# Optimization experiments

Measured on AMD Instinct MI355X. Metric: run time of the kernel, lower is better.

Reference implementation:

```python
import jax, jax.numpy as jnp
import numpy as np

N = 8192      # number of tokens/nodes
D = 256       # out_dim
E = N - 1     # one dependency triple per non-root node
ALPHA = 0.2   # LeakyReLU negative slope


def setup_inputs() -> dict:
    key = jax.random.key(0)
    k1, k2, k3, k4 = jax.random.split(key, 4)
    x = jax.random.normal(k1, (N, D), jnp.float32)
    W = jax.random.normal(k2, (D, D), jnp.float32) / np.sqrt(D)      # nn.Linear(out,out,bias=False).weight
    a = jax.random.normal(k3, (2 * D,), jnp.float32) / np.sqrt(2 * D)  # nn.Linear(2*out,1,bias=False).weight
    # each node 1..N-1 is a dependent exactly once -> h_dict keys are [0,1,...,N-1] in order
    dep = jnp.arange(1, N, dtype=jnp.int32)
    # each governor appears at most once -> each e_tensor row is softmaxed exactly once
    gov = jax.random.permutation(k4, N)[:E].astype(jnp.int32)
    return {"x": x, "W": W, "a": a, "dep": dep, "gov": gov}


def reference(x, W, a, dep, gov):
    Nn, Dd = x.shape
    neg_big = jnp.asarray(-1e18, x.dtype)
    Hx = x @ W.T  # self.weight(x[i]) for every node, [N, D]
    # per-edge attention logit: attn_weight(cat(W x_gov, W x_dep))
    s = jnp.concatenate([Hx[gov], Hx[dep]], axis=-1) @ a  # [E]
    # dense e_tensor exactly as in the module
    e = jnp.zeros((Nn, Nn), x.dtype).at[gov, dep].set(s)
    # rows belonging to a governor get masked softmax; other rows untouched
    gov_mask = jnp.zeros((Nn,), bool).at[gov].set(True)
    masked = jnp.where(e > 0, e, neg_big)
    sm = jax.nn.softmax(masked, axis=1)
    attn = jnp.where(gov_mask[:, None], sm, e)
    # self_loop/h_dict init: h[dep] = W x[gov]; node 0 stays zeros
    h = jnp.zeros((Nn, Dd), x.dtype).at[dep].set(Hx[gov])
    # aggregation: h[gov] += attn[gov, dep] * W x[dep]
    coef = attn[gov, dep]  # [E]
    h = h + jax.ops.segment_sum(coef[:, None] * Hx[dep], gov, num_segments=Nn)
    return jax.nn.leaky_relu(h, ALPHA)
```

## Files before the change

### kernel.cpp

```cpp
#include <hip/hip_runtime.h>
#include <hip/hip_bf16.h>

#define NN 8192
#define DD 256
#define EE (NN - 1)

typedef __attribute__((ext_vector_type(8))) short bf16x8;
typedef __attribute__((ext_vector_type(4))) float f32x4;

__device__ inline unsigned short f2bf(float f) {
  return __builtin_bit_cast(unsigned short, __float2bfloat16(f));
}

__global__ __launch_bounds__(1024) void prep(
    const float* __restrict__ W, const float* __restrict__ a,
    const int* __restrict__ gov,
    float* __restrict__ u, float* __restrict__ v, int* __restrict__ inv) {
  const int t = threadIdx.x;
  const int k = t & 255, part = t >> 8;

  for (int i = t; i < NN; i += 1024) inv[i] = -1;
  __syncthreads();
  for (int e = t; e < EE; e += 1024) inv[gov[e]] = e;

  float up = 0.f, vp = 0.f;
  const int j0 = part * 64;
#pragma unroll 4
  for (int j = j0; j < j0 + 64; ++j) {
    float w = W[(size_t)j * DD + k];
    up = fmaf(a[j], w, up);
    vp = fmaf(a[DD + j], w, vp);
  }
  __shared__ float redu[4][256], redv[4][256];
  redu[part][k] = up; redv[part][k] = vp;
  __syncthreads();
  if (t < 256) {
    u[t] = redu[0][t] + redu[1][t] + redu[2][t] + redu[3][t];
    v[t] = redv[0][t] + redv[1][t] + redv[2][t] + redv[3][t];
  }
}

__global__ __launch_bounds__(256) void pq_kernel(
    const float* __restrict__ x, const float* __restrict__ u,
    const float* __restrict__ v, float* __restrict__ p, float* __restrict__ q) {
  const int wid = threadIdx.x >> 6, lane = threadIdx.x & 63;
  const int row = blockIdx.x * 4 + wid;
  const float4 xv = *(const float4*)&x[(size_t)row * DD + lane * 4];
  const float4 uv = *(const float4*)&u[lane * 4];
  const float4 vv = *(const float4*)&v[lane * 4];
  float ps = xv.x * uv.x + xv.y * uv.y + xv.z * uv.z + xv.w * uv.w;
  float qs = xv.x * vv.x + xv.y * vv.y + xv.z * vv.z + xv.w * vv.w;
#pragma unroll
  for (int off = 32; off; off >>= 1) {
    ps += __shfl_xor(ps, off);
    qs += __shfl_xor(qs, off);
  }
  if (lane == 0) { p[row] = ps; q[row] = qs; }
}

__global__ __launch_bounds__(256) void combine(
    const float* __restrict__ x, const float* __restrict__ p,
    const float* __restrict__ q, const int* __restrict__ gov,
    const int* __restrict__ inv, unsigned short* __restrict__ y) {
  const int sub = threadIdx.x >> 6, lane = threadIdx.x & 63;
  const int j = blockIdx.x * 4 + sub;

  float4 h = make_float4(0.f, 0.f, 0.f, 0.f);
  if (j > 0) {
    const int g = gov[j - 1];
    h = *(const float4*)&x[(size_t)g * DD + lane * 4];
  }
  const int e2 = inv[j];
  if (e2 >= 0) {
    const int d = e2 + 1;
    const float4 xd = *(const float4*)&x[(size_t)d * DD + lane * 4];
    const float s = p[j] + q[d];
    const float coef = (s > 0.f) ? 1.f : (1.f / 8192.f);
    h.x = fmaf(coef, xd.x, h.x);
    h.y = fmaf(coef, xd.y, h.y);
    h.z = fmaf(coef, xd.z, h.z);
    h.w = fmaf(coef, xd.w, h.w);
  }
  ushort4 pk;
  pk.x = f2bf(h.x); pk.y = f2bf(h.y); pk.z = f2bf(h.z); pk.w = f2bf(h.w);
  *(ushort4*)&y[(size_t)j * DD + lane * 4] = pk;
}

#define BM 64
#define BN 64
#define BK 32
#define LDAB 40

__global__ __launch_bounds__(256) void gemm_out(
    const unsigned short* __restrict__ Y, const float* __restrict__ W,
    float* __restrict__ out) {
  __shared__ unsigned short As[BM][LDAB];
  __shared__ unsigned short Bs[BN][LDAB];
  const int t = threadIdx.x;
  const int bm = blockIdx.x * BM, bn = blockIdx.y * BN;
  const int lane = t & 63, wid = t >> 6;
  const int wr = wid >> 1, wc = wid & 1;
  const int l15 = lane & 15, l4 = lane >> 4;
  const int srow = t >> 2, sseg = t & 3;

  f32x4 acc[2][2] = {};

  for (int k0 = 0; k0 < DD; k0 += BK) {
    {
      ushort4 w0 = *(const ushort4*)&Y[(size_t)(bm + srow) * DD + k0 + sseg * 8];
      ushort4 w1 = *(const ushort4*)&Y[(size_t)(bm + srow) * DD + k0 + sseg * 8 + 4];
      *(ushort4*)&As[srow][sseg * 8] = w0;
      *(ushort4*)&As[srow][sseg * 8 + 4] = w1;
    }
    {
      const float* src = &W[(size_t)(bn + srow) * DD + k0 + sseg * 8];
      float4 f0 = *(const float4*)src;
      float4 f1 = *(const float4*)(src + 4);
      ushort4 p0, p1;
      p0.x = f2bf(f0.x); p0.y = f2bf(f0.y); p0.z = f2bf(f0.z); p0.w = f2bf(f0.w);
      p1.x = f2bf(f1.x); p1.y = f2bf(f1.y); p1.z = f2bf(f1.z); p1.w = f2bf(f1.w);
      *(ushort4*)&Bs[srow][sseg * 8] = p0;
      *(ushort4*)&Bs[srow][sseg * 8 + 4] = p1;
    }
    __syncthreads();

    bf16x8 af[2], bfr[2];
#pragma unroll
    for (int mf = 0; mf < 2; ++mf)
      af[mf] = *(const bf16x8*)&As[wr * 32 + mf * 16 + l15][l4 * 8];
#pragma unroll
    for (int nf = 0; nf < 2; ++nf)
      bfr[nf] = *(const bf16x8*)&Bs[wc * 32 + nf * 16 + l15][l4 * 8];
#pragma unroll
    for (int mf = 0; mf < 2; ++mf)
#pragma unroll
      for (int nf = 0; nf < 2; ++nf)
        acc[mf][nf] = __builtin_amdgcn_mfma_f32_16x16x32_bf16(
            af[mf], bfr[nf], acc[mf][nf], 0, 0, 0);
    __syncthreads();
  }

#pragma unroll
  for (int mf = 0; mf < 2; ++mf)
#pragma unroll
    for (int nf = 0; nf < 2; ++nf)
#pragma unroll
      for (int r = 0; r < 4; ++r) {
        const int row = bm + wr * 32 + mf * 16 + l4 * 4 + r;
        const int col = bn + wc * 32 + nf * 16 + l15;
        float hval = acc[mf][nf][r];
        out[(size_t)row * DD + col] = (hval >= 0.f) ? hval : 0.2f * hval;
      }
}

extern "C" void kernel_launch(void* const* d_in, const int* in_sizes, int n_in,
                              void* d_out, int out_size, void* d_ws, size_t ws_size,
                              hipStream_t stream) {
  const float* x = (const float*)d_in[0];
  const float* W = (const float*)d_in[1];
  const float* a = (const float*)d_in[2];
  const int* gov = (const int*)d_in[4];

  float* p = (float*)d_ws;
  float* q = p + NN;
  float* u = q + NN;
  float* v = u + DD;
  int* inv = (int*)(v + DD);
  unsigned short* y = (unsigned short*)(inv + NN);

  hipLaunchKernelGGL(prep, dim3(1), dim3(1024), 0, stream, W, a, gov, u, v, inv);
  hipLaunchKernelGGL(pq_kernel, dim3(NN / 4), dim3(256), 0, stream, x, u, v, p, q);
  hipLaunchKernelGGL(combine, dim3(NN / 4), dim3(256), 0, stream,
                     x, p, q, gov, inv, y);
  hipLaunchKernelGGL(gemm_out, dim3(NN / BM, DD / BN), dim3(256), 0, stream,
                     y, W, (float*)d_out);
}
```

Baseline: 96.94 us.

## Fuse all four stages into one cooperative persistent kernel with grid syncs

Replaces the four separate launches (prep, pq, combine, gemm) with a single cooperative kernel of 512 blocks that steps through the phases using grid.sync. The u/v projection is now split across 64 blocks with a two-level reduction instead of one 1024-thread block, which shortens the serial prep step. The p/q dot products are computed inline in the combine phase, so the separate p/q pass and its arrays go away. The aim is to cut launch gaps and the single-block bottleneck, at the cost of three grid-wide barriers and a fixed grid that must fit fully resident on the device.

```diff
diff --git a/kernel.cpp b/kernel.cpp
--- a/kernel.cpp
+++ b/kernel.cpp
@@ -1,9 +1,14 @@
 #include <hip/hip_runtime.h>
 #include <hip/hip_bf16.h>
+#include <hip/hip_cooperative_groups.h>
+
+namespace cg = cooperative_groups;
 
 #define NN 8192
 #define DD 256
 #define EE (NN - 1)
+#define NB 512
+#define NT 256
 
 typedef __attribute__((ext_vector_type(8))) short bf16x8;
 typedef __attribute__((ext_vector_type(4))) float f32x4;
@@ -12,145 +17,144 @@
   return __builtin_bit_cast(unsigned short, __float2bfloat16(f));
 }
 
-__global__ __launch_bounds__(1024) void prep(
-    const float* __restrict__ W, const float* __restrict__ a,
-    const int* __restrict__ gov,
-    float* __restrict__ u, float* __restrict__ v, int* __restrict__ inv) {
-  const int t = threadIdx.x;
-  const int k = t & 255, part = t >> 8;
-
-  for (int i = t; i < NN; i += 1024) inv[i] = -1;
-  __syncthreads();
-  for (int e = t; e < EE; e += 1024) inv[gov[e]] = e;
-
-  float up = 0.f, vp = 0.f;
-  const int j0 = part * 64;
-#pragma unroll 4
-  for (int j = j0; j < j0 + 64; ++j) {
-    float w = W[(size_t)j * DD + k];
-    up = fmaf(a[j], w, up);
-    vp = fmaf(a[DD + j], w, vp);
-  }
-  __shared__ float redu[4][256], redv[4][256];
-  redu[part][k] = up; redv[part][k] = vp;
-  __syncthreads();
-  if (t < 256) {
-    u[t] = redu[0][t] + redu[1][t] + redu[2][t] + redu[3][t];
-    v[t] = redv[0][t] + redv[1][t] + redv[2][t] + redv[3][t];
-  }
-}
-
-__global__ __launch_bounds__(256) void pq_kernel(
-    const float* __restrict__ x, const float* __restrict__ u,
-    const float* __restrict__ v, float* __restrict__ p, float* __restrict__ q) {
-  const int wid = threadIdx.x >> 6, lane = threadIdx.x & 63;
-  const int row = blockIdx.x * 4 + wid;
-  const float4 xv = *(const float4*)&x[(size_t)row * DD + lane * 4];
-  const float4 uv = *(const float4*)&u[lane * 4];
-  const float4 vv = *(const float4*)&v[lane * 4];
-  float ps = xv.x * uv.x + xv.y * uv.y + xv.z * uv.z + xv.w * uv.w;
-  float qs = xv.x * vv.x + xv.y * vv.y + xv.z * vv.z + xv.w * vv.w;
-#pragma unroll
-  for (int off = 32; off; off >>= 1) {
-    ps += __shfl_xor(ps, off);
-    qs += __shfl_xor(qs, off);
-  }
-  if (lane == 0) { p[row] = ps; q[row] = qs; }
-}
-
-__global__ __launch_bounds__(256) void combine(
-    const float* __restrict__ x, const float* __restrict__ p,
-    const float* __restrict__ q, const int* __restrict__ gov,
-    const int* __restrict__ inv, unsigned short* __restrict__ y) {
-  const int sub = threadIdx.x >> 6, lane = threadIdx.x & 63;
-  const int j = blockIdx.x * 4 + sub;
-
-  float4 h = make_float4(0.f, 0.f, 0.f, 0.f);
-  if (j > 0) {
-    const int g = gov[j - 1];
-    h = *(const float4*)&x[(size_t)g * DD + lane * 4];
-  }
-  const int e2 = inv[j];
-  if (e2 >= 0) {
-    const int d = e2 + 1;
-    const float4 xd = *(const float4*)&x[(size_t)d * DD + lane * 4];
-    const float s = p[j] + q[d];
-    const float coef = (s > 0.f) ? 1.f : (1.f / 8192.f);
-    h.x = fmaf(coef, xd.x, h.x);
-    h.y = fmaf(coef, xd.y, h.y);
-    h.z = fmaf(coef, xd.z, h.z);
-    h.w = fmaf(coef, xd.w, h.w);
-  }
-  ushort4 pk;
-  pk.x = f2bf(h.x); pk.y = f2bf(h.y); pk.z = f2bf(h.z); pk.w = f2bf(h.w);
-  *(ushort4*)&y[(size_t)j * DD + lane * 4] = pk;
-}
-
 #define BM 64
 #define BN 64
-#define BK 32
 #define LDAB 40
 
-__global__ __launch_bounds__(256) void gemm_out(
-    const unsigned short* __restrict__ Y, const float* __restrict__ W,
+__global__ __launch_bounds__(NT, 2) void fused(
+    const float* __restrict__ x, const float* __restrict__ W,
+    const float* __restrict__ a, const int* __restrict__ gov,
+    float* __restrict__ pu, float* __restrict__ pv,
+    float* __restrict__ u, float* __restrict__ v,
+    int* __restrict__ inv, unsigned short* __restrict__ y,
     float* __restrict__ out) {
+  cg::grid_group grid = cg::this_grid();
+  const int blk = blockIdx.x, t = threadIdx.x;
+
   __shared__ unsigned short As[BM][LDAB];
   __shared__ unsigned short Bs[BN][LDAB];
-  const int t = threadIdx.x;
-  const int bm = blockIdx.x * BM, bn = blockIdx.y * BN;
-  const int lane = t & 63, wid = t >> 6;
-  const int wr = wid >> 1, wc = wid & 1;
-  const int l15 = lane & 15, l4 = lane >> 4;
-  const int srow = t >> 2, sseg = t & 3;
 
-  f32x4 acc[2][2] = {};
+  if (blk < 64) {
+    float su = 0.f, sv = 0.f;
+    const int j0 = blk * 4;
+#pragma unroll
+    for (int jj = 0; jj < 4; ++jj) {
+      float w = W[(size_t)(j0 + jj) * DD + t];
+      su = fmaf(a[j0 + jj], w, su);
+      sv = fmaf(a[DD + j0 + jj], w, sv);
+    }
+    pu[blk * DD + t] = su;
+    pv[blk * DD + t] = sv;
+  } else if (blk < 96) {
+    inv[(blk - 64) * 256 + t] = -1;
+  }
+  grid.sync();
 
-  for (int k0 = 0; k0 < DD; k0 += BK) {
-    {
-      ushort4 w0 = *(const ushort4*)&Y[(size_t)(bm + srow) * DD + k0 + sseg * 8];
-      ushort4 w1 = *(const ushort4*)&Y[(size_t)(bm + srow) * DD + k0 + sseg * 8 + 4];
-      *(ushort4*)&As[srow][sseg * 8] = w0;
-      *(ushort4*)&As[srow][sseg * 8 + 4] = w1;
+  if (blk == 0) {
+    float su = 0.f, sv = 0.f;
+#pragma unroll 8
+    for (int b = 0; b < 64; ++b) {
+      su += pu[b * DD + t];
+      sv += pv[b * DD + t];
     }
-    {
-      const float* src = &W[(size_t)(bn + srow) * DD + k0 + sseg * 8];
-      float4 f0 = *(const float4*)src;
-      float4 f1 = *(const float4*)(src + 4);
-      ushort4 p0, p1;
-      p0.x = f2bf(f0.x); p0.y = f2bf(f0.y); p0.z = f2bf(f0.z); p0.w = f2bf(f0.w);
-      p1.x = f2bf(f1.x); p1.y = f2bf(f1.y); p1.z = f2bf(f1.z); p1.w = f2bf(f1.w);
-      *(ushort4*)&Bs[srow][sseg * 8] = p0;
-      *(ushort4*)&Bs[srow][sseg * 8 + 4] = p1;
+    u[t] = su;
+    v[t] = sv;
+  } else if (blk >= 96 && blk < 128) {
+    const int e = (blk - 96) * 256 + t;
+    if (e < EE) inv[gov[e]] = e;
+  }
+  grid.sync();
+
+  {
+    const int wid = t >> 6, lane = t & 63;
+    const float4 uv = *(const float4*)&u[lane * 4];
+    const float4 vv = *(const float4*)&v[lane * 4];
+#pragma unroll
+    for (int r = 0; r < 4; ++r) {
+      const int j = blk * 16 + wid * 4 + r;
+      float4 h = make_float4(0.f, 0.f, 0.f, 0.f);
+      if (j > 0) {
+        const int g = gov[j - 1];
+        h = *(const float4*)&x[(size_t)g * DD + lane * 4];
+      }
+      const int e2 = inv[j];
+      if (e2 >= 0) {
+        const int d = e2 + 1;
+        const float4 xj = *(const float4*)&x[(size_t)j * DD + lane * 4];
+        const float4 xd = *(const float4*)&x[(size_t)d * DD + lane * 4];
+        float s = xj.x * uv.x + xj.y * uv.y + xj.z * uv.z + xj.w * uv.w +
+                  xd.x * vv.x + xd.y * vv.y + xd.z * vv.z + xd.w * vv.w;
+#pragma unroll
+        for (int off = 32; off; off >>= 1) s += __shfl_xor(s, off);
+        const float coef = (s > 0.f) ? 1.f : (1.f / 8192.f);
+        h.x = fmaf(coef, xd.x, h.x);
+        h.y = fmaf(coef, xd.y, h.y);
+        h.z = fmaf(coef, xd.z, h.z);
+        h.w = fmaf(coef, xd.w, h.w);
+      }
+      ushort4 pk;
+      pk.x = f2bf(h.x); pk.y = f2bf(h.y); pk.z = f2bf(h.z); pk.w = f2bf(h.w);
+      *(ushort4*)&y[(size_t)j * DD + lane * 4] = pk;
     }
-    __syncthreads();
+  }
+  grid.sync();
 
-    bf16x8 af[2], bfr[2];
+  {
+    const int bm = (blk & 127) * BM, bn = (blk >> 7) * BN;
+    const int lane = t & 63, wid = t >> 6;
+    const int wr = wid >> 1, wc = wid & 1;
+    const int l15 = lane & 15, l4 = lane >> 4;
+    const int srow = t >> 2, sseg = t & 3;
+
+    f32x4 acc[2][2] = {};
+
+    for (int k0 = 0; k0 < DD; k0 += 32) {
+      {
+        ushort4 w0 = *(const ushort4*)&y[(size_t)(bm + srow) * DD + k0 + sseg * 8];
+        ushort4 w1 = *(const ushort4*)&y[(size_t)(bm + srow) * DD + k0 + sseg * 8 + 4];
+        *(ushort4*)&As[srow][sseg * 8] = w0;
+        *(ushort4*)&As[srow][sseg * 8 + 4] = w1;
+      }
+      {
+        const float* src = &W[(size_t)(bn + srow) * DD + k0 + sseg * 8];
+        float4 f0 = *(const float4*)src;
+        float4 f1 = *(const float4*)(src + 4);
+        ushort4 p0, p1;
+        p0.x = f2bf(f0.x); p0.y = f2bf(f0.y); p0.z = f2bf(f0.z); p0.w = f2bf(f0.w);
+        p1.x = f2bf(f1.x); p1.y = f2bf(f1.y); p1.z = f2bf(f1.z); p1.w = f2bf(f1.w);
+        *(ushort4*)&Bs[srow][sseg * 8] = p0;
+        *(ushort4*)&Bs[srow][sseg * 8 + 4] = p1;
+      }
+      __syncthreads();
+
+      bf16x8 af[2], bfr[2];
 #pragma unroll
-    for (int mf = 0; mf < 2; ++mf)
-      af[mf] = *(const bf16x8*)&As[wr * 32 + mf * 16 + l15][l4 * 8];
+      for (int mf = 0; mf < 2; ++mf)
+        af[mf] = *(const bf16x8*)&As[wr * 32 + mf * 16 + l15][l4 * 8];
 #pragma unroll
-    for (int nf = 0; nf < 2; ++nf)
-      bfr[nf] = *(const bf16x8*)&Bs[wc * 32 + nf * 16 + l15][l4 * 8];
+      for (int nf = 0; nf < 2; ++nf)
+        bfr[nf] = *(const bf16x8*)&Bs[wc * 32 + nf * 16 + l15][l4 * 8];
+#pragma unroll
+      for (int mf = 0; mf < 2; ++mf)
+#pragma unroll
+        for (int nf = 0; nf < 2; ++nf)
+          acc[mf][nf] = __builtin_amdgcn_mfma_f32_16x16x32_bf16(
+              af[mf], bfr[nf], acc[mf][nf], 0, 0, 0);
+      __syncthreads();
+    }
+
 #pragma unroll
     for (int mf = 0; mf < 2; ++mf)
 #pragma unroll
       for (int nf = 0; nf < 2; ++nf)
-        acc[mf][nf] = __builtin_amdgcn_mfma_f32_16x16x32_bf16(
-            af[mf], bfr[nf], acc[mf][nf], 0, 0, 0);
-    __syncthreads();
+#pragma unroll
+        for (int r = 0; r < 4; ++r) {
+          const int row = bm + wr * 32 + mf * 16 + l4 * 4 + r;
+          const int col = bn + wc * 32 + nf * 16 + l15;
+          float hval = acc[mf][nf][r];
+          out[(size_t)row * DD + col] = (hval >= 0.f) ? hval : 0.2f * hval;
+        }
   }
-
-#pragma unroll
-  for (int mf = 0; mf < 2; ++mf)
-#pragma unroll
-    for (int nf = 0; nf < 2; ++nf)
-#pragma unroll
-      for (int r = 0; r < 4; ++r) {
-        const int row = bm + wr * 32 + mf * 16 + l4 * 4 + r;
-        const int col = bn + wc * 32 + nf * 16 + l15;
-        float hval = acc[mf][nf][r];
-        out[(size_t)row * DD + col] = (hval >= 0.f) ? hval : 0.2f * hval;
-      }
 }
 
 extern "C" void kernel_launch(void* const* d_in, const int* in_sizes, int n_in,
@@ -161,17 +165,17 @@
   const float* a = (const float*)d_in[2];
   const int* gov = (const int*)d_in[4];
 
-  float* p = (float*)d_ws;
-  float* q = p + NN;
-  float* u = q + NN;
-  float* v = u + DD;
-  int* inv = (int*)(v + DD);
+  float* pu = (float*)d_ws;
+  float* pv = pu + 64 * DD;
+  float* u  = pv + 64 * DD;
+  float* v  = u + DD;
+  int* inv  = (int*)(v + DD);
   unsigned short* y = (unsigned short*)(inv + NN);
+  float* outp = (float*)d_out;
 
-  hipLaunchKernelGGL(prep, dim3(1), dim3(1024), 0, stream, W, a, gov, u, v, inv);
-  hipLaunchKernelGGL(pq_kernel, dim3(NN / 4), dim3(256), 0, stream, x, u, v, p, q);
-  hipLaunchKernelGGL(combine, dim3(NN / 4), dim3(256), 0, stream,
-                     x, p, q, gov, inv, y);
-  hipLaunchKernelGGL(gemm_out, dim3(NN / BM, DD / BN), dim3(256), 0, stream,
-                     y, W, (float*)d_out);
+  void* args[] = {(void*)&x, (void*)&W, (void*)&a, (void*)&gov,
+                  (void*)&pu, (void*)&pv, (void*)&u, (void*)&v,
+                  (void*)&inv, (void*)&y, (void*)&outp};
+  hipLaunchCooperativeKernel((const void*)fused, dim3(NB), dim3(NT), args, 0,
+                             stream);
 }
```

New measurement: 247.5 us. 2.55x slower.
